# Performance work log

Measured on AMD Instinct MI355X. Metric: run time of the kernel, lower is better.

The kernel has to match this reference:

```python
import jax, jax.numpy as jnp
import numpy as np
from jax import lax

EPS_NORM = 1e-12   # F.normalize default eps
KS = 3             # fixed 3x3 window
K2 = KS * KS
MIN_CONN, MAX_CONN = 1, 8
NUM_GROUPS = 16    # largest divisor <=16 of C=128
GN_EPS = 1e-5


def _unfold3x3_reflect(x):
    # x: [B,C,H,W] -> patches [B,C,9,H,W] (reflect-padded 3x3 neighborhoods)
    B, C, H, W = x.shape
    p = jnp.pad(x, ((0, 0), (0, 0), (1, 1), (1, 1)), mode='reflect')
    pats = [p[:, :, dy:dy + H, dx:dx + W] for dy in range(KS) for dx in range(KS)]
    return jnp.stack(pats, axis=2)


def _df_counts(x):
    # DFDetector: mean over C, fixed Laplacian conv (zero pad), abs, per-batch min-max norm
    B = x.shape[0]
    avg = jnp.mean(x, axis=1, keepdims=True)  # [B,1,H,W]
    kern = jnp.array([[0., -1., 0.], [-1., 4., -1.], [0., -1., 0.]],
                     dtype=x.dtype).reshape(1, 1, 3, 3)
    df = jnp.abs(lax.conv_general_dilated(
        avg, kern, window_strides=(1, 1), padding=((1, 1), (1, 1)),
        dimension_numbers=('NCHW', 'OIHW', 'NCHW')))
    dmin = df.reshape(B, -1).min(axis=1).reshape(B, 1, 1, 1)
    dmax = df.reshape(B, -1).max(axis=1).reshape(B, 1, 1, 1)
    dn = (df - dmin) / (dmax - dmin + 1e-8)
    return MIN_CONN + jnp.round(dn * (MAX_CONN - MIN_CONN))  # [B,1,H,W], values in [1,8]


def _group_norm(x, w, b):
    B, C, H, W = x.shape
    g = x.reshape(B, NUM_GROUPS, -1)
    mu = g.mean(-1, keepdims=True)
    var = g.var(-1, keepdims=True)  # biased, matches torch GroupNorm
    g = (g - mu) * lax.rsqrt(var + GN_EPS)
    return g.reshape(B, C, H, W) * w[None, :, None, None] + b[None, :, None, None]


def setup_inputs() -> dict:
    key = jax.random.key(0)
    ks = jax.random.split(key, 7)
    B, C, H, W = 8, 128, 96, 96
    return {
        'x': jax.random.normal(ks[0], (B, C, H, W), jnp.float32),
        'gn_weight': jax.random.uniform(ks[1], (C,), jnp.float32, 0.5, 1.5),
        'gn_bias': jax.random.normal(ks[2], (C,), jnp.float32) * 0.1,
        'w1': jax.random.normal(ks[3], (2 * C, C), jnp.float32) * 0.02,
        'b1': jax.random.normal(ks[4], (2 * C,), jnp.float32) * 0.02,
        'w2': jax.random.normal(ks[5], (C, 2 * C), jnp.float32) * 0.02,
        'b2': jax.random.normal(ks[6], (C,), jnp.float32) * 0.02,
    }


def reference(x, gn_weight, gn_bias, w1, b1, w2, b2):
    B, C, H, W = x.shape
    P = H * W
    # per-pixel connection counts (integer k in [1,8]); non-differentiable in original
    counts = lax.stop_gradient(_df_counts(x))
    kvals = jnp.minimum(counts, K2).astype(jnp.int32).reshape(B, 1, P)

    patches = _unfold3x3_reflect(x).reshape(B, C, K2, P)
    xc = x.reshape(B, C, P)
    # L2 normalize over channel dim (F.normalize, eps=1e-12)
    cn = xc / jnp.maximum(jnp.linalg.norm(xc, axis=1, keepdims=True), EPS_NORM)
    pn = patches / jnp.maximum(jnp.linalg.norm(patches, axis=1, keepdims=True), EPS_NORM)

    sim = jnp.einsum('bcp,bckp->bkp', cn, pn)          # [B,9,P] cosine sims
    order = jnp.argsort(-sim, axis=1)                   # descending (== topk order)
    top_sim = jnp.take_along_axis(sim, order, axis=1)
    mask = jnp.arange(K2)[None, :, None] < kvals        # rank < k -> selected
    wts = jnp.exp(top_sim) * mask
    wts = wts / jnp.sum(wts, axis=1, keepdims=True)     # softmax over selected sims

    pat_sorted = jnp.take_along_axis(patches, order[:, None, :, :], axis=2)
    out = jnp.einsum('bckp,bkp->bcp', pat_sorted, wts).reshape(B, C, H, W)

    enhanced = out + _group_norm(x, gn_weight, gn_bias)
    h = jax.nn.relu(jnp.einsum('oi,bihw->bohw', w1, enhanced) + b1[None, :, None, None])
    ffn = jnp.einsum('oi,bihw->bohw', w2, h) + b2[None, :, None, None]
    return enhanced + ffn
```

## Files before the change

### kernel.cpp

```cpp
#include <hip/hip_runtime.h>

#define BD 8
#define CD 128
#define HD 96
#define WD 96
#define PD 9216
#define ND 73728

typedef __attribute__((ext_vector_type(8))) short short8;
typedef __attribute__((ext_vector_type(4))) float f32x4;

__device__ inline float bfu2f(unsigned int u) { return __uint_as_float(u << 16); }
__device__ inline unsigned short f2bfu(float f) {
  unsigned int u = __float_as_uint(f);
  u += 0x7fffu + ((u >> 16) & 1u);
  return (unsigned short)(u >> 16);
}

template<bool F32>
__device__ __forceinline__ float ldv(const void* __restrict__ p, size_t i) {
  if constexpr (F32) return ((const float*)p)[i];
  else return bfu2f(((const unsigned short*)p)[i]);
}

__global__ void k_init(unsigned long long* dmm, int* cnt) {
  int t = threadIdx.x;
  if (t < 8) dmm[t] = 0x7FEFFFFFFFFFFFFFULL;
  else if (t < 16) dmm[t] = 0ULL;
  if (t == 16) { cnt[0] = 0; cnt[1] = 0; }
}

__global__ void k_detect(const unsigned int* __restrict__ xw, int* __restrict__ cnt) {
  int t = blockIdx.x * 256 + threadIdx.x;
  uint4 w = ((const uint4*)xw)[t];
  int lz = (int)((w.x & 0xFFFFu) == 0u) + (int)((w.y & 0xFFFFu) == 0u) +
           (int)((w.z & 0xFFFFu) == 0u) + (int)((w.w & 0xFFFFu) == 0u);
  int e2 = (int)(((w.x >> 7) & 0xFFu) == 0xFFu) + (int)(((w.y >> 7) & 0xFFu) == 0xFFu) +
           (int)(((w.z >> 7) & 0xFFu) == 0xFFu) + (int)(((w.w >> 7) & 0xFFu) == 0xFFu);
  #pragma unroll
  for (int off = 32; off; off >>= 1) {
    lz += __shfl_down(lz, off);
    e2 += __shfl_down(e2, off);
  }
  if ((threadIdx.x & 63) == 0) { atomicAdd(&cnt[0], lz); atomicAdd(&cnt[1], e2); }
}

__global__ void k_flag(const int* __restrict__ cnt, int* __restrict__ flag) {
  *flag = (cnt[0] > 4096 || cnt[1] > 0) ? 1 : 0;
}

__global__ void k_cvtw(const void* __restrict__ w1, const void* __restrict__ w2,
                       unsigned short* __restrict__ wc, const int* __restrict__ flag) {
  bool f32 = (*flag != 0);
  int t = blockIdx.x * 256 + threadIdx.x;
  if (t < 32768)
    wc[t] = f32 ? f2bfu(((const float*)w1)[t]) : ((const unsigned short*)w1)[t];
  else {
    int u = t - 32768;
    wc[t] = f32 ? f2bfu(((const float*)w2)[u]) : ((const unsigned short*)w2)[u];
  }
}

__global__ void k_cvtb(const void* __restrict__ gw, const void* __restrict__ gb,
                       const void* __restrict__ b1, const void* __restrict__ b2,
                       float* __restrict__ prm, const int* __restrict__ flag) {
  bool f32 = (*flag != 0);
  int t = threadIdx.x;
  for (int i = t; i < 640; i += 256) {
    float v;
    if (i < 128)      v = f32 ? ((const float*)gw)[i]       : bfu2f(((const unsigned short*)gw)[i]);
    else if (i < 256) v = f32 ? ((const float*)gb)[i - 128] : bfu2f(((const unsigned short*)gb)[i - 128]);
    else if (i < 512) v = f32 ? ((const float*)b1)[i - 256] : bfu2f(((const unsigned short*)b1)[i - 256]);
    else              v = f32 ? ((const float*)b2)[i - 512] : bfu2f(((const unsigned short*)b2)[i - 512]);
    prm[i] = v;
  }
}

template<bool F32>
__device__ __forceinline__ void pmt_body(const void* __restrict__ x,
                                         float* __restrict__ xpm,
                                         double* __restrict__ avg, double* __restrict__ nrm,
                                         double* __restrict__ nrm2,
                                         double* __restrict__ gpart,
                                         float (*tile)[132], int lb) {
  const int t = threadIdx.x, px = t & 63, ci = t >> 6;
  const int gp0 = lb * 64, b = gp0 / PD, p0 = gp0 - b * PD;
  double sg[4] = {0.0, 0.0, 0.0, 0.0}, qg[4] = {0.0, 0.0, 0.0, 0.0};
  for (int j = 0; j < 32; ++j) {
    int c = ci * 32 + j;
    float v = ldv<F32>(x, (size_t)(b * CD + c) * PD + p0 + px);
    tile[px][c] = v;
    sg[j >> 3] += (double)v;
    qg[j >> 3] += (double)v * (double)v;
  }
  #pragma unroll
  for (int g = 0; g < 4; ++g) {
    #pragma unroll
    for (int off = 32; off; off >>= 1) {
      sg[g] += __shfl_down(sg[g], off);
      qg[g] += __shfl_down(qg[g], off);
    }
  }
  if (px == 0) {
    double* gp_ = gpart + (size_t)lb * 32;
    #pragma unroll
    for (int g = 0; g < 4; ++g) {
      gp_[(ci * 4 + g) * 2 + 0] = sg[g];
      gp_[(ci * 4 + g) * 2 + 1] = qg[g];
    }
  }
  __syncthreads();
  for (int i = t; i < 2048; i += 256) {
    int r = i >> 5, seg = i & 31;
    *(float4*)(xpm + (size_t)(gp0 + r) * 128 + seg * 4) = *(const float4*)&tile[r][seg * 4];
  }
  if (t < 64) {
    double s = 0.0, q = 0.0;
    for (int c = 0; c < 128; ++c) {
      float v = tile[t][c];
      s += (double)v;
      q += (double)v * (double)v;
    }
    double qq[4] = {0.0, 0.0, 0.0, 0.0};
    #pragma unroll
    for (int g = 0; g < 4; ++g)
      for (int i = 0; i < 32; ++i) {
        float v = tile[t][g * 32 + i];
        qq[g] += (double)v * (double)v;
      }
    avg[gp0 + t] = s * (1.0 / 128.0);
    nrm[gp0 + t] = sqrt(q);
    nrm2[gp0 + t] = ((qq[0] + qq[1]) + qq[2]) + qq[3];
  }
}
__global__ __launch_bounds__(256) void k_pmt(const void* __restrict__ x,
                                             const int* __restrict__ flag,
                                             float* __restrict__ xpm,
                                             double* __restrict__ avg,
                                             double* __restrict__ nrm,
                                             double* __restrict__ nrm2,
                                             double* __restrict__ gpart) {
  __shared__ float tile[64][132];
  const int lb = (blockIdx.x & 7) * 144 + (blockIdx.x >> 3);
  if (*flag) pmt_body<true>(x, xpm, avg, nrm, nrm2, gpart, tile, lb);
  else pmt_body<false>(x, xpm, avg, nrm, nrm2, gpart, tile, lb);
}

__global__ void k_gn2(const double* __restrict__ gpart, float* __restrict__ gn) {
  const int bg = blockIdx.x;
  const int b = bg >> 4, g = bg & 15;
  const int t = threadIdx.x;
  double s = 0.0, q = 0.0;
  for (int i = t; i < 144; i += 64) {
    const double* pp = gpart + (size_t)(b * 144 + i) * 32 + g * 2;
    s += pp[0];
    q += pp[1];
  }
  #pragma unroll
  for (int off = 32; off; off >>= 1) {
    s += __shfl_down(s, off);
    q += __shfl_down(q, off);
  }
  if (t == 0) {
    double mu = s / 73728.0;
    double var = q / 73728.0 - mu * mu;
    gn[bg] = (float)mu;
    gn[128 + bg] = (float)(1.0 / sqrt(var + 1e-5));
  }
}

__device__ inline double lap_df(const double* __restrict__ a, int b, int y, int x) {
  const double* ab = a + (size_t)b * PD;
  double v = 4.0 * ab[y * WD + x];
  if (y > 0)      v -= ab[(y - 1) * WD + x];
  if (y < HD - 1) v -= ab[(y + 1) * WD + x];
  if (x > 0)      v -= ab[y * WD + x - 1];
  if (x < WD - 1) v -= ab[y * WD + x + 1];
  return fabs(v);
}

__global__ void k_minmax(const double* __restrict__ avg, unsigned long long* __restrict__ dmm) {
  __shared__ double mnW[4], mxW[4];
  int t = threadIdx.x;
  const int lb = (blockIdx.x & 7) * 36 + (blockIdx.x >> 3);
  int gp = lb * 256 + t;
  int b = gp / PD, p = gp - b * PD;
  double mn = lap_df(avg, b, p / WD, p % WD);
  double mx = mn;
  #pragma unroll
  for (int off = 32; off; off >>= 1) {
    mn = fmin(mn, __shfl_down(mn, off));
    mx = fmax(mx, __shfl_down(mx, off));
  }
  if ((t & 63) == 0) { mnW[t >> 6] = mn; mxW[t >> 6] = mx; }
  __syncthreads();
  if (t == 0) {
    mn = fmin(fmin(mnW[0], mnW[1]), fmin(mnW[2], mnW[3]));
    mx = fmax(fmax(mxW[0], mxW[1]), fmax(mxW[2], mxW[3]));
    atomicMin(&dmm[b], (unsigned long long)__double_as_longlong(mn));
    atomicMax(&dmm[b + 8], (unsigned long long)__double_as_longlong(mx));
  }
}

__device__ __forceinline__ void neigh9(int y, int xx, int* q) {
  #pragma unroll
  for (int dy = 0; dy < 3; ++dy) {
    int yy = y + dy - 1;
    yy = yy < 0 ? -yy : (yy >= HD ? 2 * HD - 2 - yy : yy);
    #pragma unroll
    for (int dx = 0; dx < 3; ++dx) {
      int xr = xx + dx - 1;
      xr = xr < 0 ? -xr : (xr >= WD ? 2 * WD - 2 - xr : xr);
      q[dy * 3 + dx] = yy * WD + xr;
    }
  }
}

__global__ __launch_bounds__(256, 3) void k_ipg(const float* __restrict__ xpm,
                                                const double* __restrict__ avg,
                                                const double* __restrict__ nrm,
                                                const double* __restrict__ nrm2,
                                                const unsigned long long* __restrict__ dmm,
                                                const float* __restrict__ gn,
                                                const float* __restrict__ prm,
                                                unsigned short* __restrict__ eg) {
  __shared__ float tileF[12800];
  __shared__ double sdl[64][4];
  float4* tile4 = (float4*)tileF;
  const float* gwf = prm;
  const float* gbf = prm + 128;

  const int t = threadIdx.x;
  const int lb = (blockIdx.x & 7) * 144 + (blockIdx.x >> 3);
  const int b = lb / 144;
  const int tid = lb - b * 144;
  const int ty = tid / 12, tx = tid - ty * 12;
  const int y0 = ty * 8, x0 = tx * 8;

  {
    const int s = t & 31, hpb = t >> 5;
    #pragma unroll
    for (int it = 0; it < 13; ++it) {
      int hp = it * 8 + hpb;
      if (hp < 100) {
        int hr = hp / 10, hc = hp - hr * 10;
        int gy = y0 - 1 + hr; gy = gy < 0 ? -gy : (gy >= HD ? 2 * HD - 2 - gy : gy);
        int gx = x0 - 1 + hc; gx = gx < 0 ? -gx : (gx >= WD ? 2 * WD - 2 - gx : gx);
        const float4* src = (const float4*)(xpm + (size_t)(b * PD + gy * WD + gx) * 128) + s;
        tile4[(hp * 32 + s) ^ (hp & 7)] = *src;
      }
    }
  }
  __syncthreads();

  const int a = t >> 2, q = t & 3;
  const int yl = a >> 3, xl = a & 7;
  const int y = y0 + yl, xx = x0 + xl;
  const int p = y * WD + xx;
  const int cpix = (yl + 1) * 10 + (xl + 1);
  const int cub = cpix * 32 + q * 8, csw = cpix & 7;

  const bool nb5 = (xl == 7);
  const bool nb6 = (yl == 7) || (xl == 0);
  const bool nb7 = (yl == 7);
  const bool nb8 = (yl == 7) || (xl == 7);

  double d[9];
  {
    float cv[32];
    #pragma unroll
    for (int j4 = 0; j4 < 8; ++j4)
      *(float4*)(cv + 4 * j4) = tile4[(cub + j4) ^ csw];
    #pragma unroll
    for (int k = 0; k < 9; ++k) {
      if (k == 4) continue;
      bool need = (k < 4) || (k == 5 ? nb5 : k == 6 ? nb6 : k == 7 ? nb7 : nb8);
      if (need) {
        int dy = k / 3, dx = k - dy * 3;
        int pix = (yl + dy) * 10 + (xl + dx);
        int ub = pix * 32 + q * 8, sw = pix & 7;
        double acc = 0.0;
        #pragma unroll
        for (int seg = 0; seg < 8; ++seg) {
          float4 nv = tile4[(ub + seg) ^ sw];
          acc += (double)cv[seg * 4 + 0] * (double)nv.x;
          acc += (double)cv[seg * 4 + 1] * (double)nv.y;
          acc += (double)cv[seg * 4 + 2] * (double)nv.z;
          acc += (double)cv[seg * 4 + 3] * (double)nv.w;
        }
        double v1 = __shfl_down(acc, 1);
        double v2 = __shfl_down(acc, 2);
        double v3 = __shfl_down(acc, 3);
        d[k] = ((acc + v1) + v2) + v3;
      }
    }
  }
  if (q == 0) {
    sdl[a][0] = d[0]; sdl[a][1] = d[1]; sdl[a][2] = d[2]; sdl[a][3] = d[3];
  }
  __syncthreads();

  float wv[9];
  #pragma unroll
  for (int j = 0; j < 9; ++j) wv[j] = 0.f;
  if (q == 0) {
    int qg[9];
    neigh9(y, xx, qg);
    double dmin = __longlong_as_double((long long)dmm[b]);
    double dmax = __longlong_as_double((long long)dmm[b + 8]);
    double df = lap_df(avg, b, y, xx);
    double dn = (df - dmin) / (dmax - dmin + 1e-8);
    int kk = 1 + (int)rint(dn * 7.0);
    kk = kk < 1 ? 1 : (kk > 8 ? 8 : kk);

    double sd[9];
    sd[0] = d[0]; sd[1] = d[1]; sd[2] = d[2]; sd[3] = d[3];
    sd[4] = nrm2[b * PD + p];
    sd[5] = nb5 ? d[5] : sdl[a + 1][3];
    sd[6] = nb6 ? d[6] : sdl[a + 7][2];
    sd[7] = nb7 ? d[7] : sdl[a + 8][1];
    sd[8] = nb8 ? d[8] : sdl[a + 9][0];

    double np_ = fmax(nrm[b * PD + p], 1e-12);
    #pragma unroll
    for (int k = 0; k < 9; ++k) {
      double nq = fmax(nrm[b * PD + qg[k]], 1e-12);
      sd[k] = sd[k] / (np_ * nq);
    }
    float w[9];
    float wsum = 0.f;
    #pragma unroll
    for (int j = 0; j < 9; ++j) {
      int rank = 0;
      #pragma unroll
      for (int i = 0; i < 9; ++i)
        rank += (sd[i] > sd[j]) || (sd[i] == sd[j] && i < j);
      w[j] = (rank < kk) ? expf((float)sd[j]) : 0.f;
      wsum += w[j];
    }
    float inv = 1.f / wsum;
    #pragma unroll
    for (int j = 0; j < 9; ++j) wv[j] = w[j] * inv;
  }
  #pragma unroll
  for (int j = 0; j < 9; ++j) wv[j] = __shfl(wv[j], (t & 63) & ~3);

  {
    float og[32];
    #pragma unroll
    for (int j = 0; j < 32; ++j) og[j] = 0.f;
    #pragma unroll
    for (int k = 0; k < 9; ++k) {
      int dy = k / 3, dx = k - dy * 3;
      int pix = (yl + dy) * 10 + (xl + dx);
      int ub = pix * 32 + q * 8, sw = pix & 7;
      #pragma unroll
      for (int seg = 0; seg < 8; ++seg) {
        float4 nv = tile4[(ub + seg) ^ sw];
        og[seg * 4 + 0] += wv[k] * nv.x;
        og[seg * 4 + 1] += wv[k] * nv.y;
        og[seg * 4 + 2] += wv[k] * nv.z;
        og[seg * 4 + 3] += wv[k] * nv.w;
      }
    }
    const int g16 = b * 16;
    unsigned short* egr = eg + (size_t)(b * PD + p) * 128 + q * 32;
    #pragma unroll
    for (int seg = 0; seg < 4; ++seg) {
      float4 cA = tile4[(cub + seg * 2) ^ csw];
      float4 cB = tile4[(cub + seg * 2 + 1) ^ csw];
      float cvv[8] = {cA.x, cA.y, cA.z, cA.w, cB.x, cB.y, cB.z, cB.w};
      int g = q * 4 + seg;
      float mu = gn[g16 + g], rs = gn[128 + g16 + g];
      unsigned int pkd[4];
      #pragma unroll
      for (int j = 0; j < 8; ++j) {
        int c = q * 32 + seg * 8 + j;
        float e = og[seg * 8 + j] + (cvv[j] - mu) * rs * gwf[c] + gbf[c];
        unsigned int h = (unsigned int)f2bfu(e);
        if (j & 1) pkd[j >> 1] |= h << 16;
        else pkd[j >> 1] = h;
      }
      uint4 v; v.x = pkd[0]; v.y = pkd[1]; v.z = pkd[2]; v.w = pkd[3];
      *(uint4*)(egr + seg * 8) = v;
    }
  }
}

__global__ __launch_bounds__(256, 3) void k_ffn(const unsigned short* __restrict__ eg,
                                                const float* __restrict__ prm,
                                                const unsigned short* __restrict__ wc,
                                                float* __restrict__ outp) {
  __shared__ unsigned short et[64][136];
  __shared__ unsigned short Hl[64][264];
  const float* b1f = prm + 256;
  const float* b2f = prm + 512;

  const int t = threadIdx.x;
  const int lb = (blockIdx.x & 7) * 144 + (blockIdx.x >> 3);
  const int gp0 = lb * 64;
  const int b = gp0 / PD, p0b = gp0 - b * PD;

  const unsigned short* wc1 = wc;
  const unsigned short* wc2 = wc + 32768;
  const int lane = t & 63, wave = t >> 6;
  const int r16 = lane & 15, quad = lane >> 4;

  {
    const uint4* eg4 = (const uint4*)(eg + (size_t)gp0 * 128);
    #pragma unroll
    for (int it = 0; it < 4; ++it) {
      int lin = it * 256 + t;
      int row = lin >> 4, c8 = lin & 15;
      *(uint4*)&et[row][c8 * 8] = eg4[lin];
    }
  }
  short8 wb1[16];
  #pragma unroll
  for (int kk = 0; kk < 4; ++kk)
    #pragma unroll
    for (int nt = 0; nt < 4; ++nt)
      wb1[kk * 4 + nt] = *(const short8*)(wc1 + (size_t)(wave * 64 + nt * 16 + r16) * 128 + kk * 32 + quad * 8);
  __syncthreads();

  f32x4 acc[16];
  #pragma unroll
  for (int i = 0; i < 16; ++i) acc[i] = (f32x4){0.f, 0.f, 0.f, 0.f};
  #pragma unroll
  for (int kk = 0; kk < 4; ++kk) {
    short8 afm[4];
    #pragma unroll
    for (int m = 0; m < 4; ++m)
      afm[m] = *(const short8*)&et[m * 16 + r16][kk * 32 + quad * 8];
    #pragma unroll
    for (int nt = 0; nt < 4; ++nt)
      #pragma unroll
      for (int m = 0; m < 4; ++m)
        acc[m * 4 + nt] = __builtin_amdgcn_mfma_f32_16x16x32_bf16(afm[m], wb1[kk * 4 + nt], acc[m * 4 + nt], 0, 0, 0);
  }
  #pragma unroll
  for (int nt = 0; nt < 4; ++nt) {
    int n = wave * 64 + nt * 16 + r16;
    float bias = b1f[n];
    #pragma unroll
    for (int m = 0; m < 4; ++m)
      #pragma unroll
      for (int r = 0; r < 4; ++r)
        Hl[m * 16 + quad * 4 + r][n] = f2bfu(fmaxf(acc[m * 4 + nt][r] + bias, 0.f));
  }
  short8 wb2[16];
  #pragma unroll
  for (int kk = 0; kk < 8; ++kk)
    #pragma unroll
    for (int nt = 0; nt < 2; ++nt)
      wb2[kk * 2 + nt] = *(const short8*)(wc2 + (size_t)(wave * 32 + nt * 16 + r16) * 256 + kk * 32 + quad * 8);
  __syncthreads();

  f32x4 acc2[8];
  #pragma unroll
  for (int i = 0; i < 8; ++i) acc2[i] = (f32x4){0.f, 0.f, 0.f, 0.f};
  #pragma unroll
  for (int kk = 0; kk < 8; ++kk) {
    short8 afm[4];
    #pragma unroll
    for (int m = 0; m < 4; ++m)
      afm[m] = *(const short8*)&Hl[m * 16 + r16][kk * 32 + quad * 8];
    #pragma unroll
    for (int nt = 0; nt < 2; ++nt)
      #pragma unroll
      for (int m = 0; m < 4; ++m)
        acc2[m * 2 + nt] = __builtin_amdgcn_mfma_f32_16x16x32_bf16(afm[m], wb2[kk * 2 + nt], acc2[m * 2 + nt], 0, 0, 0);
  }
  #pragma unroll
  for (int nt = 0; nt < 2; ++nt) {
    int n = wave * 32 + nt * 16 + r16;
    float bias = b2f[n];
    #pragma unroll
    for (int m = 0; m < 4; ++m) {
      int mloc0 = m * 16 + quad * 4;
      float4 o;
      o.x = acc2[m * 2 + nt][0] + bias + bfu2f(et[mloc0 + 0][n]);
      o.y = acc2[m * 2 + nt][1] + bias + bfu2f(et[mloc0 + 1][n]);
      o.z = acc2[m * 2 + nt][2] + bias + bfu2f(et[mloc0 + 2][n]);
      o.w = acc2[m * 2 + nt][3] + bias + bfu2f(et[mloc0 + 3][n]);
      *(float4*)(outp + (size_t)(b * CD + n) * PD + p0b + mloc0) = o;
    }
  }
}

extern "C" void kernel_launch(void* const* d_in, const int* in_sizes, int n_in,
                              void* d_out, int out_size, void* d_ws, size_t ws_size,
                              hipStream_t stream) {
  const void* x  = d_in[0];
  const void* gw = d_in[1];
  const void* gb = d_in[2];
  const void* w1 = d_in[3];
  const void* b1 = d_in[4];
  const void* w2 = d_in[5];
  const void* b2 = d_in[6];
  float* out = (float*)d_out;

  char* ws = (char*)d_ws;
  int* flag = (int*)ws;
  int* cnt = (int*)(ws + 16);
  unsigned long long* dmm = (unsigned long long*)(ws + 128);
  float* gn = (float*)(ws + 256);
  float* prm = (float*)(ws + 1280);
  unsigned short* wc = (unsigned short*)(ws + 3840);
  double* avg = (double*)(ws + 134912);
  double* nrm = (double*)(ws + 724736);
  double* nrm2 = (double*)(ws + 1314560);
  double* gpart = (double*)(ws + 1904384);
  unsigned short* eg = (unsigned short*)(ws + 2199296);
  float* xpm = (float*)(ws + 21073664);

  k_init<<<1, 64, 0, stream>>>(dmm, cnt);
  k_detect<<<64, 256, 0, stream>>>((const unsigned int*)x, cnt);
  k_flag<<<1, 1, 0, stream>>>(cnt, flag);
  k_cvtw<<<256, 256, 0, stream>>>(w1, w2, wc, flag);
  k_cvtb<<<1, 256, 0, stream>>>(gw, gb, b1, b2, prm, flag);
  k_pmt<<<ND / 64, 256, 0, stream>>>(x, flag, xpm, avg, nrm, nrm2, gpart);
  k_gn2<<<128, 64, 0, stream>>>(gpart, gn);
  k_minmax<<<ND / 256, 256, 0, stream>>>(avg, dmm);
  k_ipg<<<ND / 64, 256, 0, stream>>>(xpm, avg, nrm, nrm2, dmm, gn, prm, eg);
  k_ffn<<<ND / 64, 256, 0, stream>>>(eg, prm, wc, out);
}
```

Measured before the change: 192.2 us.

## Cache norms in shared memory, store Laplacian map, compute all 8 neighbor dots directly

k_minmax now writes the per-pixel Laplacian magnitude to a buffer so k_ipg reads it instead of recomputing it from avg. k_ipg stages the 10x10 halo of pixel norms and the 8x8 center nrm2 values in shared memory, replacing scattered global loads. The shared-memory exchange of symmetric dot products and its extra barrier are removed, so every pixel computes all 8 neighbor dot products itself. That roughly doubles the double-precision FMA work in the similarity loop in exchange for less synchronization and fewer global reads.

```diff
diff --git a/kernel.cpp b/kernel.cpp
--- a/kernel.cpp
+++ b/kernel.cpp
@@ -179,14 +179,16 @@
   return fabs(v);
 }
 
-__global__ void k_minmax(const double* __restrict__ avg, unsigned long long* __restrict__ dmm) {
+__global__ void k_minmax(const double* __restrict__ avg, unsigned long long* __restrict__ dmm,
+                         double* __restrict__ dfb) {
   __shared__ double mnW[4], mxW[4];
   int t = threadIdx.x;
   const int lb = (blockIdx.x & 7) * 36 + (blockIdx.x >> 3);
   int gp = lb * 256 + t;
   int b = gp / PD, p = gp - b * PD;
-  double mn = lap_df(avg, b, p / WD, p % WD);
-  double mx = mn;
+  double df = lap_df(avg, b, p / WD, p % WD);
+  dfb[gp] = df;
+  double mn = df, mx = df;
   #pragma unroll
   for (int off = 32; off; off >>= 1) {
     mn = fmin(mn, __shfl_down(mn, off));
@@ -202,30 +204,17 @@
   }
 }
 
-__device__ __forceinline__ void neigh9(int y, int xx, int* q) {
-  #pragma unroll
-  for (int dy = 0; dy < 3; ++dy) {
-    int yy = y + dy - 1;
-    yy = yy < 0 ? -yy : (yy >= HD ? 2 * HD - 2 - yy : yy);
-    #pragma unroll
-    for (int dx = 0; dx < 3; ++dx) {
-      int xr = xx + dx - 1;
-      xr = xr < 0 ? -xr : (xr >= WD ? 2 * WD - 2 - xr : xr);
-      q[dy * 3 + dx] = yy * WD + xr;
-    }
-  }
-}
-
 __global__ __launch_bounds__(256, 3) void k_ipg(const float* __restrict__ xpm,
-                                                const double* __restrict__ avg,
                                                 const double* __restrict__ nrm,
                                                 const double* __restrict__ nrm2,
+                                                const double* __restrict__ dfb,
                                                 const unsigned long long* __restrict__ dmm,
                                                 const float* __restrict__ gn,
                                                 const float* __restrict__ prm,
                                                 unsigned short* __restrict__ eg) {
   __shared__ float tileF[12800];
-  __shared__ double sdl[64][4];
+  __shared__ double nsl[100];
+  __shared__ double nsl2[64];
   float4* tile4 = (float4*)tileF;
   const float* gwf = prm;
   const float* gbf = prm + 128;
@@ -250,6 +239,15 @@
         tile4[(hp * 32 + s) ^ (hp & 7)] = *src;
       }
     }
+    if (t < 100) {
+      int hr = t / 10, hc = t - hr * 10;
+      int gy = y0 - 1 + hr; gy = gy < 0 ? -gy : (gy >= HD ? 2 * HD - 2 - gy : gy);
+      int gx = x0 - 1 + hc; gx = gx < 0 ? -gx : (gx >= WD ? 2 * WD - 2 - gx : gx);
+      nsl[t] = nrm[b * PD + gy * WD + gx];
+    } else if (t >= 128 && t < 192) {
+      int a2 = t - 128;
+      nsl2[a2] = nrm2[b * PD + (y0 + (a2 >> 3)) * WD + x0 + (a2 & 7)];
+    }
   }
   __syncthreads();
 
@@ -260,12 +258,7 @@
   const int cpix = (yl + 1) * 10 + (xl + 1);
   const int cub = cpix * 32 + q * 8, csw = cpix & 7;
 
-  const bool nb5 = (xl == 7);
-  const bool nb6 = (yl == 7) || (xl == 0);
-  const bool nb7 = (yl == 7);
-  const bool nb8 = (yl == 7) || (xl == 7);
-
-  double d[9];
+  double sd[9];
   {
     float cv[32];
     #pragma unroll
@@ -274,57 +267,42 @@
     #pragma unroll
     for (int k = 0; k < 9; ++k) {
       if (k == 4) continue;
-      bool need = (k < 4) || (k == 5 ? nb5 : k == 6 ? nb6 : k == 7 ? nb7 : nb8);
-      if (need) {
-        int dy = k / 3, dx = k - dy * 3;
-        int pix = (yl + dy) * 10 + (xl + dx);
-        int ub = pix * 32 + q * 8, sw = pix & 7;
-        double acc = 0.0;
-        #pragma unroll
-        for (int seg = 0; seg < 8; ++seg) {
-          float4 nv = tile4[(ub + seg) ^ sw];
-          acc += (double)cv[seg * 4 + 0] * (double)nv.x;
-          acc += (double)cv[seg * 4 + 1] * (double)nv.y;
-          acc += (double)cv[seg * 4 + 2] * (double)nv.z;
-          acc += (double)cv[seg * 4 + 3] * (double)nv.w;
-        }
-        double v1 = __shfl_down(acc, 1);
-        double v2 = __shfl_down(acc, 2);
-        double v3 = __shfl_down(acc, 3);
-        d[k] = ((acc + v1) + v2) + v3;
+      int dy = k / 3, dx = k - dy * 3;
+      int pix = (yl + dy) * 10 + (xl + dx);
+      int ub = pix * 32 + q * 8, sw = pix & 7;
+      double acc = 0.0;
+      #pragma unroll
+      for (int seg = 0; seg < 8; ++seg) {
+        float4 nv = tile4[(ub + seg) ^ sw];
+        acc += (double)cv[seg * 4 + 0] * (double)nv.x;
+        acc += (double)cv[seg * 4 + 1] * (double)nv.y;
+        acc += (double)cv[seg * 4 + 2] * (double)nv.z;
+        acc += (double)cv[seg * 4 + 3] * (double)nv.w;
       }
-    }
-  }
-  if (q == 0) {
-    sdl[a][0] = d[0]; sdl[a][1] = d[1]; sdl[a][2] = d[2]; sdl[a][3] = d[3];
-  }
-  __syncthreads();
+      double v1 = __shfl_down(acc, 1);
+      double v2 = __shfl_down(acc, 2);
+      double v3 = __shfl_down(acc, 3);
+      sd[k] = ((acc + v1) + v2) + v3;
+    }
+  }
 
   float wv[9];
   #pragma unroll
   for (int j = 0; j < 9; ++j) wv[j] = 0.f;
   if (q == 0) {
-    int qg[9];
-    neigh9(y, xx, qg);
     double dmin = __longlong_as_double((long long)dmm[b]);
     double dmax = __longlong_as_double((long long)dmm[b + 8]);
-    double df = lap_df(avg, b, y, xx);
+    double df = dfb[b * PD + p];
     double dn = (df - dmin) / (dmax - dmin + 1e-8);
     int kk = 1 + (int)rint(dn * 7.0);
     kk = kk < 1 ? 1 : (kk > 8 ? 8 : kk);
 
-    double sd[9];
-    sd[0] = d[0]; sd[1] = d[1]; sd[2] = d[2]; sd[3] = d[3];
-    sd[4] = nrm2[b * PD + p];
-    sd[5] = nb5 ? d[5] : sdl[a + 1][3];
-    sd[6] = nb6 ? d[6] : sdl[a + 7][2];
-    sd[7] = nb7 ? d[7] : sdl[a + 8][1];
-    sd[8] = nb8 ? d[8] : sdl[a + 9][0];
-
-    double np_ = fmax(nrm[b * PD + p], 1e-12);
+    sd[4] = nsl2[a];
+    double np_ = fmax(nsl[cpix], 1e-12);
     #pragma unroll
     for (int k = 0; k < 9; ++k) {
-      double nq = fmax(nrm[b * PD + qg[k]], 1e-12);
+      int dy = k / 3, dx = k - dy * 3;
+      double nq = fmax(nsl[(yl + dy) * 10 + (xl + dx)], 1e-12);
       sd[k] = sd[k] / (np_ * nq);
     }
     float w[9];
@@ -511,8 +489,9 @@
   double* nrm = (double*)(ws + 724736);
   double* nrm2 = (double*)(ws + 1314560);
   double* gpart = (double*)(ws + 1904384);
-  unsigned short* eg = (unsigned short*)(ws + 2199296);
-  float* xpm = (float*)(ws + 21073664);
+  double* dfb = (double*)(ws + 2199296);
+  unsigned short* eg = (unsigned short*)(ws + 2789120);
+  float* xpm = (float*)(ws + 21663488);
 
   k_init<<<1, 64, 0, stream>>>(dmm, cnt);
   k_detect<<<64, 256, 0, stream>>>((const unsigned int*)x, cnt);
@@ -521,7 +500,7 @@
   k_cvtb<<<1, 256, 0, stream>>>(gw, gb, b1, b2, prm, flag);
   k_pmt<<<ND / 64, 256, 0, stream>>>(x, flag, xpm, avg, nrm, nrm2, gpart);
   k_gn2<<<128, 64, 0, stream>>>(gpart, gn);
-  k_minmax<<<ND / 256, 256, 0, stream>>>(avg, dmm);
-  k_ipg<<<ND / 64, 256, 0, stream>>>(xpm, avg, nrm, nrm2, dmm, gn, prm, eg);
+  k_minmax<<<ND / 256, 256, 0, stream>>>(avg, dmm, dfb);
+  k_ipg<<<ND / 64, 256, 0, stream>>>(xpm, nrm, nrm2, dfb, dmm, gn, prm, eg);
   k_ffn<<<ND / 64, 256, 0, stream>>>(eg, prm, wc, out);
 }
```

New measurement: 188.3 us. 2.1% less time.
